# Optimization experiments

Hardware: AMD Instinct MI355X
Metric: run time of the kernel (lower is better)

Reference implementation:

```python
import jax, jax.numpy as jnp
import numpy as np

K = 3          # kernel_size
DIL = 2        # dilation
PAD = 2        # padding = dilation*(K-1)/2 so output spatial == input spatial
RANKS = 3
EPS = 1e-6


def _unfold(h):
    """Replicate-pad then extract KxK dilated patches -> (b, c, K*K, H, W).
    Kernel-position ordering matches torch.nn.Unfold (row-major kh*K+kw)."""
    b, c, H, W = h.shape
    p = jnp.pad(h, ((0, 0), (0, 0), (PAD, PAD), (PAD, PAD)), mode='edge')
    patches = [p[:, :, i * DIL:i * DIL + H, j * DIL:j * DIL + W]
               for i in range(K) for j in range(K)]
    return jnp.stack(patches, axis=2)  # (b, c, K*K, H, W)


def setup_inputs() -> dict:
    key = jax.random.key(0)
    k1, k2, k3 = jax.random.split(key, 3)
    B, C, H, W = 4, 64, 128, 128
    x = jax.random.normal(k1, (B, C, H, W), dtype=jnp.float32)
    W_head = jax.random.normal(k2, (64, 64), dtype=jnp.float32) * 0.05  # (out_c, in_c)
    W_tail = jax.random.normal(k3, (64, 64), dtype=jnp.float32) * 0.05  # (in_c, out_c)
    return {"x": x, "W_head": W_head, "W_tail": W_tail}


def reference(x, W_head, W_tail):
    res = x
    # 1x1 head conv (no bias) + ReLU
    h = jax.nn.relu(jnp.einsum('oc,bchw->bohw', W_head, x))
    # im2col: (b, C, K*K, H, W)
    X = _unfold(h)
    # NMF-style init: broadcast means over kernel / channel dims to rank r
    U = jnp.repeat(X.mean(axis=2, keepdims=True), RANKS, axis=2)  # (b,c,r,h,w)
    V = jnp.repeat(X.mean(axis=1, keepdims=True), RANKS, axis=1)  # (b,r,k,h,w)
    # one Lee-Seung multiplicative update (stage_num=1)
    num = jnp.einsum('bcrhw,bckhw->brkhw', U, X)
    den = jnp.einsum('bcrhw,bckhw->brkhw', U,
                     jnp.einsum('bcrhw,brkhw->bckhw', U, V))
    V = V * (num / (den + EPS))
    num = jnp.einsum('bckhw,brkhw->bcrhw', X, V)
    den = jnp.einsum('bckhw,brkhw->bcrhw',
                     jnp.einsum('bcrhw,brkhw->bckhw', U, V), V)
    U = U * (num / (den + EPS))
    center = (K // 2) * K + K // 2  # = 4
    UV = jnp.einsum('bcrhw,brkhw->bckhw', U, V[:, :, center:center + 1])[:, :, 0]
    out = jnp.einsum('co,bohw->bchw', W_tail, UV) + res
    return out
```

## Files before the change

### kernel.cpp

```cpp
#include <hip/hip_runtime.h>
#include <hip/hip_bf16.h>

#define HWC 16384
#define WD  128
#define NC  64
#define EPSV 1e-6f

typedef __attribute__((ext_vector_type(8))) short bf16x8;
typedef __attribute__((ext_vector_type(4))) float f32x4;
typedef __attribute__((ext_vector_type(2))) float f32x2;
typedef __attribute__((ext_vector_type(4))) unsigned int u32x4;

__device__ __forceinline__ unsigned cvt2(float a, float b) {
  union { __hip_bfloat162 h; unsigned u; } r;
  r.h = __float22bfloat162_rn(make_float2(a, b));
  return r.u;
}
__device__ __forceinline__ float bfLo(unsigned pk) { return __builtin_bit_cast(float, pk << 16); }
__device__ __forceinline__ float bfHi(unsigned pk) { return __builtin_bit_cast(float, pk & 0xFFFF0000u); }
__device__ __forceinline__ f32x2 up2(unsigned w) {
  f32x2 r; r[0] = bfLo(w); r[1] = bfHi(w); return r;
}
__device__ __forceinline__ float frcp(float x) { return __builtin_amdgcn_rcpf(x); }
__device__ __forceinline__ int swz(int row, int colbytes) {
  return ((row << 7) + colbytes) ^ ((row & 7) << 4);
}
__device__ __forceinline__ bf16x8 pack8(float4 a, float4 b) {
  union { unsigned u[4]; bf16x8 v; } r;
  r.u[0] = cvt2(a.x, a.y); r.u[1] = cvt2(a.z, a.w);
  r.u[2] = cvt2(b.x, b.y); r.u[3] = cvt2(b.z, b.w);
  return r.v;
}

__global__ __launch_bounds__(512) void k_fused(const float* __restrict__ x,
                                               const float* __restrict__ Wh,
                                               const float* __restrict__ Wt,
                                               float* __restrict__ out) {
  __shared__ __align__(16) char smem[53248];
  unsigned short* xt = (unsigned short*)smem;
  unsigned short* hl = (unsigned short*)(smem + 26624);
  unsigned short* uvb = (unsigned short*)smem;

  const int t = threadIdx.x, lane = t & 63, wv = t >> 6;
  const int bid0 = blockIdx.x;
  const int bid = ((bid0 & 7) << 7) | (bid0 >> 3);
  const int seg = bid & 1, y = (bid >> 1) & 127, b = bid >> 8;
  const int w0 = seg << 6;
  const int c0 = wv << 3;
  const int l15 = lane & 15, kg = lane >> 4;
  const int mt = wv & 3;
  const int mrow = (mt << 4) + l15;

  int gy[3];
  gy[0] = y >= 2 ? y - 2 : 0;
  gy[1] = y;
  gy[2] = y <= 125 ? y + 2 : 127;

  const float* xb = x + (size_t)b * (NC * HWC);

  bf16x8 ha0, ha1;
  {
    const float* wr = Wh + mrow * 64 + kg * 8;
    ha0 = pack8(*(const float4*)wr, *(const float4*)(wr + 4));
    ha1 = pack8(*(const float4*)(wr + 32), *(const float4*)(wr + 36));
  }

  {
    int colm = w0 - 2 + lane; if (colm < 0) colm = 0;
#pragma unroll
    for (int r = 0; r < 3; ++r) {
      const float* xr = xb + gy[r] * WD + colm;
      float f[8];
#pragma unroll
      for (int u = 0; u < 8; ++u) f[u] = xr[(size_t)(c0 + u) * HWC];
      u32x4 v;
      v[0] = cvt2(f[0], f[1]); v[1] = cvt2(f[2], f[3]);
      v[2] = cvt2(f[4], f[5]); v[3] = cvt2(f[6], f[7]);
      *(u32x4*)((char*)xt + swz(r * 68 + lane, c0 * 2)) = v;
    }
    if (lane < 12) {
      const int re = lane >> 2, e = lane & 3;
      int cole = w0 + 62 + e; if (cole > 127) cole = 127;
      const float* xr = xb + gy[re] * WD + cole;
      float f[8];
#pragma unroll
      for (int u = 0; u < 8; ++u) f[u] = xr[(size_t)(c0 + u) * HWC];
      u32x4 v;
      v[0] = cvt2(f[0], f[1]); v[1] = cvt2(f[2], f[3]);
      v[2] = cvt2(f[4], f[5]); v[3] = cvt2(f[6], f[7]);
      *(u32x4*)((char*)xt + swz(re * 68 + 64 + e, c0 * 2)) = v;
    }
  }
  __syncthreads();

  {
    const int ntBeg = (wv >> 2) ? 7 : 0;
    const int ntEnd = (wv >> 2) ? 13 : 7;
    const f32x4 z = {0.f, 0.f, 0.f, 0.f};
    for (int nt = ntBeg; nt < ntEnd; ++nt) {
      const int s = (nt << 4) + l15;
      const bf16x8 b0 = *(const bf16x8*)((char*)xt + swz(s, kg * 16));
      const bf16x8 b1 = *(const bf16x8*)((char*)xt + swz(s, 64 + kg * 16));
      f32x4 acc = __builtin_amdgcn_mfma_f32_16x16x32_bf16(ha0, b0, z, 0, 0, 0);
      acc = __builtin_amdgcn_mfma_f32_16x16x32_bf16(ha1, b1, acc, 0, 0, 0);
      const float v0 = acc[0] > 0.f ? acc[0] : 0.f;
      const float v1 = acc[1] > 0.f ? acc[1] : 0.f;
      const float v2 = acc[2] > 0.f ? acc[2] : 0.f;
      const float v3 = acc[3] > 0.f ? acc[3] : 0.f;
      uint2 pk2;
      pk2.x = cvt2(v0, v1);
      pk2.y = cvt2(v2, v3);
      *(uint2*)((char*)hl + swz(s, (mt * 16 + kg * 4) * 2)) = pk2;
    }
  }
  __syncthreads();

  const int px = (wv << 3) | (lane >> 3);
  const int cg16 = (lane & 7) << 4;

  u32x4 tap[9];
#pragma unroll
  for (int r = 0; r < 3; ++r)
#pragma unroll
    for (int kc = 0; kc < 3; ++kc)
      tap[r * 3 + kc] = *(const u32x4*)((char*)hl + swz(r * 68 + px + 2 * kc, cg16));

  f32x2 S2 = {0.f, 0.f};
  f32x2 sumk2[9], A2[9], mreg2[4];
#pragma unroll
  for (int k = 0; k < 9; ++k) { sumk2[k] = (f32x2){0.f, 0.f}; A2[k] = (f32x2){0.f, 0.f}; }
#pragma unroll
  for (int p = 0; p < 4; ++p) {
    f32x2 t2[9];
#pragma unroll
    for (int k = 0; k < 9; ++k) t2[k] = up2(tap[k][p]);
    f32x2 mm = t2[0];
#pragma unroll
    for (int k = 1; k < 9; ++k) mm += t2[k];
    mm *= (1.f / 9.f);
    mreg2[p] = mm;
    S2 += mm * mm;
#pragma unroll
    for (int k = 0; k < 9; ++k) { sumk2[k] += t2[k]; A2[k] += mm * t2[k]; }
  }
  float S = S2[0] + S2[1];
  float sumk[9], A[9];
#pragma unroll
  for (int k = 0; k < 9; ++k) { sumk[k] = sumk2[k][0] + sumk2[k][1]; A[k] = A2[k][0] + A2[k][1]; }

#pragma unroll
  for (int d = 1; d <= 4; d <<= 1) {
    S += __shfl_xor(S, d);
#pragma unroll
    for (int k = 0; k < 9; ++k) sumk[k] += __shfl_xor(sumk[k], d);
#pragma unroll
    for (int k = 0; k < 9; ++k) A[k] += __shfl_xor(A[k], d);
  }

  float Vk[9], T = 0.f;
#pragma unroll
  for (int k = 0; k < 9; ++k) {
    const float nk = sumk[k] * (1.f / 64.f);
    Vk[k] = nk * A[k] * frcp(3.f * nk * S + EPSV);
    T += Vk[k] * Vk[k];
  }
  const float V4 = Vk[4];

  bf16x8 ta0, ta1;
  {
    const float* wr = Wt + mrow * 64 + kg * 8;
    ta0 = pack8(*(const float4*)wr, *(const float4*)(wr + 4));
    ta1 = pack8(*(const float4*)(wr + 32), *(const float4*)(wr + 36));
  }

  {
    u32x4 uvw;
#pragma unroll
    for (int p = 0; p < 4; ++p) {
      f32x2 B2 = {0.f, 0.f};
#pragma unroll
      for (int k = 0; k < 9; ++k) B2 += up2(tap[k][p]) * Vk[k];
      const f32x2 mm = mreg2[p];
      f32x2 rden;
      rden[0] = frcp(3.f * mm[0] * T + EPSV);
      rden[1] = frcp(3.f * mm[1] * T + EPSV);
      const f32x2 Uc = mm * B2 * rden;
      const f32x2 uvv = 3.f * Uc * V4;
      uvw[p] = cvt2(uvv[0], uvv[1]);
    }
    *(u32x4*)((char*)uvb + swz(px, cg16)) = uvw;
  }
  __syncthreads();

  const int n0 = (wv >> 2) << 1;
  const f32x4 z2 = {0.f, 0.f, 0.f, 0.f};
  const size_t gb = (size_t)b * (NC * HWC) + (size_t)y * WD + w0;
#pragma unroll
  for (int nt = n0; nt < n0 + 2; ++nt) {
    const int pxs = (nt << 4) + l15;
    const bf16x8 b0 = *(const bf16x8*)((char*)uvb + swz(pxs, kg * 16));
    const bf16x8 b1 = *(const bf16x8*)((char*)uvb + swz(pxs, 64 + kg * 16));
    f32x4 acc = __builtin_amdgcn_mfma_f32_16x16x32_bf16(ta0, b0, z2, 0, 0, 0);
    acc = __builtin_amdgcn_mfma_f32_16x16x32_bf16(ta1, b1, acc, 0, 0, 0);
#pragma unroll
    for (int j = 0; j < 4; ++j) {
      const int c2 = (mt << 4) + kg * 4 + j;
      const size_t off = gb + (size_t)c2 * HWC + pxs;
      out[off] = acc[j] + x[off];
    }
  }
}

extern "C" void kernel_launch(void* const* d_in, const int* in_sizes, int n_in,
                              void* d_out, int out_size, void* d_ws, size_t ws_size,
                              hipStream_t stream) {
  const float* x  = (const float*)d_in[0];
  const float* Wh = (const float*)d_in[1];
  const float* Wt = (const float*)d_in[2];
  float* out = (float*)d_out;

  k_fused<<<1024, 512, 0, stream>>>(x, Wh, Wt, out);
}
```

Before: 24.15 us.

## Tile four output rows per block with double-buffered row staging

Each block now computes a 4-row by 32-column tile instead of one 64-wide row. It stages the 8 needed input rows one at a time into double-buffered LDS and runs the head 1x1 conv per row while the next row loads. This cuts redundant recomputation of the head conv for halo rows: it is computed 8 times per 4 outputs instead of 3 times per output. In exchange the halo overhead in width grows, there are more barriers and a serialized row loop, the launch drops to 512 blocks of 256 threads, and the ragged-tile handling adds some wasted MFMA work.

```diff
diff --git a/kernel.cpp b/kernel.cpp
--- a/kernel.cpp
+++ b/kernel.cpp
@@ -32,29 +32,59 @@
   return r.v;
 }
 
-__global__ __launch_bounds__(512) void k_fused(const float* __restrict__ x,
+__device__ __forceinline__ void stage_row(const float* __restrict__ xr, int w0,
+                                          int t, unsigned short* buf) {
+  {
+    const int s = t & 31, cg = t >> 5;
+    int col = w0 - 2 + s; if (col < 0) col = 0;
+    const float* p = xr + col;
+    float f[8];
+#pragma unroll
+    for (int u = 0; u < 8; ++u) f[u] = p[(size_t)(cg * 8 + u) * HWC];
+    u32x4 v;
+    v[0] = cvt2(f[0], f[1]); v[1] = cvt2(f[2], f[3]);
+    v[2] = cvt2(f[4], f[5]); v[3] = cvt2(f[6], f[7]);
+    *(u32x4*)((char*)buf + swz(s, cg * 16)) = v;
+  }
+  if (t < 32) {
+    const int s = 32 + (t & 3), cg = t >> 2;
+    int col = w0 - 2 + s; if (col > 127) col = 127;
+    const float* p = xr + col;
+    float f[8];
+#pragma unroll
+    for (int u = 0; u < 8; ++u) f[u] = p[(size_t)(cg * 8 + u) * HWC];
+    u32x4 v;
+    v[0] = cvt2(f[0], f[1]); v[1] = cvt2(f[2], f[3]);
+    v[2] = cvt2(f[4], f[5]); v[3] = cvt2(f[6], f[7]);
+    *(u32x4*)((char*)buf + swz(s, cg * 16)) = v;
+  }
+}
+
+__global__ __launch_bounds__(256) void k_fused(const float* __restrict__ x,
                                                const float* __restrict__ Wh,
                                                const float* __restrict__ Wt,
                                                float* __restrict__ out) {
-  __shared__ __align__(16) char smem[53248];
-  unsigned short* xt = (unsigned short*)smem;
-  unsigned short* hl = (unsigned short*)(smem + 26624);
+  __shared__ __align__(16) char smem[49152];
+  unsigned short* bufA = (unsigned short*)smem;
+  unsigned short* bufB = (unsigned short*)(smem + 6144);
+  unsigned short* hl = (unsigned short*)(smem + 12288);
   unsigned short* uvb = (unsigned short*)smem;
 
   const int t = threadIdx.x, lane = t & 63, wv = t >> 6;
   const int bid0 = blockIdx.x;
-  const int bid = ((bid0 & 7) << 7) | (bid0 >> 3);
-  const int seg = bid & 1, y = (bid >> 1) & 127, b = bid >> 8;
-  const int w0 = seg << 6;
-  const int c0 = wv << 3;
+  const int bidS = ((bid0 & 7) << 6) | (bid0 >> 3);
+  const int seg = bidS & 3, yq = (bidS >> 2) & 31, b = bidS >> 7;
+  const int w0 = seg << 5;
+  const int y0 = yq << 2;
   const int l15 = lane & 15, kg = lane >> 4;
-  const int mt = wv & 3;
-  const int mrow = (mt << 4) + l15;
-
-  int gy[3];
-  gy[0] = y >= 2 ? y - 2 : 0;
-  gy[1] = y;
-  gy[2] = y <= 125 ? y + 2 : 127;
+  const int mrow = (wv << 4) + l15;
+
+  int gyw[8];
+#pragma unroll
+  for (int i = 0; i < 8; ++i) {
+    int yy = y0 - 2 + i;
+    gyw[i] = yy < 0 ? 0 : (yy > 127 ? 127 : yy);
+  }
 
   const float* xb = x + (size_t)b * (NC * HWC);
 
@@ -65,106 +95,36 @@
     ha1 = pack8(*(const float4*)(wr + 32), *(const float4*)(wr + 36));
   }
 
-  {
-    int colm = w0 - 2 + lane; if (colm < 0) colm = 0;
-#pragma unroll
-    for (int r = 0; r < 3; ++r) {
-      const float* xr = xb + gy[r] * WD + colm;
-      float f[8];
-#pragma unroll
-      for (int u = 0; u < 8; ++u) f[u] = xr[(size_t)(c0 + u) * HWC];
-      u32x4 v;
-      v[0] = cvt2(f[0], f[1]); v[1] = cvt2(f[2], f[3]);
-      v[2] = cvt2(f[4], f[5]); v[3] = cvt2(f[6], f[7]);
-      *(u32x4*)((char*)xt + swz(r * 68 + lane, c0 * 2)) = v;
-    }
-    if (lane < 12) {
-      const int re = lane >> 2, e = lane & 3;
-      int cole = w0 + 62 + e; if (cole > 127) cole = 127;
-      const float* xr = xb + gy[re] * WD + cole;
-      float f[8];
-#pragma unroll
-      for (int u = 0; u < 8; ++u) f[u] = xr[(size_t)(c0 + u) * HWC];
-      u32x4 v;
-      v[0] = cvt2(f[0], f[1]); v[1] = cvt2(f[2], f[3]);
-      v[2] = cvt2(f[4], f[5]); v[3] = cvt2(f[6], f[7]);
-      *(u32x4*)((char*)xt + swz(re * 68 + 64 + e, c0 * 2)) = v;
-    }
-  }
+  stage_row(xb + gyw[0] * WD, w0, t, bufA);
   __syncthreads();
-
-  {
-    const int ntBeg = (wv >> 2) ? 7 : 0;
-    const int ntEnd = (wv >> 2) ? 13 : 7;
-    const f32x4 z = {0.f, 0.f, 0.f, 0.f};
-    for (int nt = ntBeg; nt < ntEnd; ++nt) {
-      const int s = (nt << 4) + l15;
-      const bf16x8 b0 = *(const bf16x8*)((char*)xt + swz(s, kg * 16));
-      const bf16x8 b1 = *(const bf16x8*)((char*)xt + swz(s, 64 + kg * 16));
-      f32x4 acc = __builtin_amdgcn_mfma_f32_16x16x32_bf16(ha0, b0, z, 0, 0, 0);
-      acc = __builtin_amdgcn_mfma_f32_16x16x32_bf16(ha1, b1, acc, 0, 0, 0);
-      const float v0 = acc[0] > 0.f ? acc[0] : 0.f;
-      const float v1 = acc[1] > 0.f ? acc[1] : 0.f;
-      const float v2 = acc[2] > 0.f ? acc[2] : 0.f;
-      const float v3 = acc[3] > 0.f ? acc[3] : 0.f;
-      uint2 pk2;
-      pk2.x = cvt2(v0, v1);
-      pk2.y = cvt2(v2, v3);
-      *(uint2*)((char*)hl + swz(s, (mt * 16 + kg * 4) * 2)) = pk2;
-    }
-  }
-  __syncthreads();
-
-  const int px = (wv << 3) | (lane >> 3);
-  const int cg16 = (lane & 7) << 4;
-
-  u32x4 tap[9];
-#pragma unroll
-  for (int r = 0; r < 3; ++r)
-#pragma unroll
-    for (int kc = 0; kc < 3; ++kc)
-      tap[r * 3 + kc] = *(const u32x4*)((char*)hl + swz(r * 68 + px + 2 * kc, cg16));
-
-  f32x2 S2 = {0.f, 0.f};
-  f32x2 sumk2[9], A2[9], mreg2[4];
-#pragma unroll
-  for (int k = 0; k < 9; ++k) { sumk2[k] = (f32x2){0.f, 0.f}; A2[k] = (f32x2){0.f, 0.f}; }
-#pragma unroll
-  for (int p = 0; p < 4; ++p) {
-    f32x2 t2[9];
-#pragma unroll
-    for (int k = 0; k < 9; ++k) t2[k] = up2(tap[k][p]);
-    f32x2 mm = t2[0];
-#pragma unroll
-    for (int k = 1; k < 9; ++k) mm += t2[k];
-    mm *= (1.f / 9.f);
-    mreg2[p] = mm;
-    S2 += mm * mm;
-#pragma unroll
-    for (int k = 0; k < 9; ++k) { sumk2[k] += t2[k]; A2[k] += mm * t2[k]; }
-  }
-  float S = S2[0] + S2[1];
-  float sumk[9], A[9];
-#pragma unroll
-  for (int k = 0; k < 9; ++k) { sumk[k] = sumk2[k][0] + sumk2[k][1]; A[k] = A2[k][0] + A2[k][1]; }
-
-#pragma unroll
-  for (int d = 1; d <= 4; d <<= 1) {
-    S += __shfl_xor(S, d);
-#pragma unroll
-    for (int k = 0; k < 9; ++k) sumk[k] += __shfl_xor(sumk[k], d);
-#pragma unroll
-    for (int k = 0; k < 9; ++k) A[k] += __shfl_xor(A[k], d);
-  }
-
-  float Vk[9], T = 0.f;
-#pragma unroll
-  for (int k = 0; k < 9; ++k) {
-    const float nk = sumk[k] * (1.f / 64.f);
-    Vk[k] = nk * A[k] * frcp(3.f * nk * S + EPSV);
-    T += Vk[k] * Vk[k];
-  }
-  const float V4 = Vk[4];
+#pragma unroll
+  for (int r = 0; r < 8; ++r) {
+    unsigned short* cur = (r & 1) ? bufB : bufA;
+    unsigned short* nxt = (r & 1) ? bufA : bufB;
+    if (r < 7) stage_row(xb + gyw[r + 1] * WD, w0, t, nxt);
+    {
+      const f32x4 zz = {0.f, 0.f, 0.f, 0.f};
+#pragma unroll
+      for (int nt = 0; nt < 3; ++nt) {
+        const int s = (nt << 4) + l15;
+        const bf16x8 b0 = *(const bf16x8*)((char*)cur + swz(s, kg * 16));
+        const bf16x8 b1 = *(const bf16x8*)((char*)cur + swz(s, 64 + kg * 16));
+        f32x4 acc = __builtin_amdgcn_mfma_f32_16x16x32_bf16(ha0, b0, zz, 0, 0, 0);
+        acc = __builtin_amdgcn_mfma_f32_16x16x32_bf16(ha1, b1, acc, 0, 0, 0);
+        if (s < 36) {
+          const float v0 = acc[0] > 0.f ? acc[0] : 0.f;
+          const float v1 = acc[1] > 0.f ? acc[1] : 0.f;
+          const float v2 = acc[2] > 0.f ? acc[2] : 0.f;
+          const float v3 = acc[3] > 0.f ? acc[3] : 0.f;
+          uint2 pk2;
+          pk2.x = cvt2(v0, v1);
+          pk2.y = cvt2(v2, v3);
+          *(uint2*)((char*)hl + swz(r * 36 + s, (wv * 16 + kg * 4) * 2)) = pk2;
+        }
+      }
+    }
+    __syncthreads();
+  }
 
   bf16x8 ta0, ta1;
   {
@@ -173,41 +133,97 @@
     ta1 = pack8(*(const float4*)(wr + 32), *(const float4*)(wr + 36));
   }
 
-  {
-    u32x4 uvw;
+  const int px = (wv << 3) | (lane >> 3);
+  const int cg16 = (lane & 7) << 4;
+
+#pragma unroll
+  for (int q = 0; q < 4; ++q) {
+    u32x4 tap[9];
+#pragma unroll
+    for (int rr = 0; rr < 3; ++rr)
+#pragma unroll
+      for (int kc = 0; kc < 3; ++kc)
+        tap[rr * 3 + kc] =
+            *(const u32x4*)((char*)hl + swz((q + 2 * rr) * 36 + px + 2 * kc, cg16));
+
+    f32x2 S2 = {0.f, 0.f};
+    f32x2 sumk2[9], A2[9], mreg2[4];
+#pragma unroll
+    for (int k = 0; k < 9; ++k) { sumk2[k] = (f32x2){0.f, 0.f}; A2[k] = (f32x2){0.f, 0.f}; }
 #pragma unroll
     for (int p = 0; p < 4; ++p) {
-      f32x2 B2 = {0.f, 0.f};
-#pragma unroll
-      for (int k = 0; k < 9; ++k) B2 += up2(tap[k][p]) * Vk[k];
-      const f32x2 mm = mreg2[p];
-      f32x2 rden;
-      rden[0] = frcp(3.f * mm[0] * T + EPSV);
-      rden[1] = frcp(3.f * mm[1] * T + EPSV);
-      const f32x2 Uc = mm * B2 * rden;
-      const f32x2 uvv = 3.f * Uc * V4;
-      uvw[p] = cvt2(uvv[0], uvv[1]);
-    }
-    *(u32x4*)((char*)uvb + swz(px, cg16)) = uvw;
-  }
-  __syncthreads();
-
-  const int n0 = (wv >> 2) << 1;
-  const f32x4 z2 = {0.f, 0.f, 0.f, 0.f};
-  const size_t gb = (size_t)b * (NC * HWC) + (size_t)y * WD + w0;
-#pragma unroll
-  for (int nt = n0; nt < n0 + 2; ++nt) {
-    const int pxs = (nt << 4) + l15;
-    const bf16x8 b0 = *(const bf16x8*)((char*)uvb + swz(pxs, kg * 16));
-    const bf16x8 b1 = *(const bf16x8*)((char*)uvb + swz(pxs, 64 + kg * 16));
-    f32x4 acc = __builtin_amdgcn_mfma_f32_16x16x32_bf16(ta0, b0, z2, 0, 0, 0);
-    acc = __builtin_amdgcn_mfma_f32_16x16x32_bf16(ta1, b1, acc, 0, 0, 0);
-#pragma unroll
-    for (int j = 0; j < 4; ++j) {
-      const int c2 = (mt << 4) + kg * 4 + j;
-      const size_t off = gb + (size_t)c2 * HWC + pxs;
-      out[off] = acc[j] + x[off];
-    }
+      f32x2 t2[9];
+#pragma unroll
+      for (int k = 0; k < 9; ++k) t2[k] = up2(tap[k][p]);
+      f32x2 mm = t2[0];
+#pragma unroll
+      for (int k = 1; k < 9; ++k) mm += t2[k];
+      mm *= (1.f / 9.f);
+      mreg2[p] = mm;
+      S2 += mm * mm;
+#pragma unroll
+      for (int k = 0; k < 9; ++k) { sumk2[k] += t2[k]; A2[k] += mm * t2[k]; }
+    }
+    float S = S2[0] + S2[1];
+    float sumk[9], A[9];
+#pragma unroll
+    for (int k = 0; k < 9; ++k) { sumk[k] = sumk2[k][0] + sumk2[k][1]; A[k] = A2[k][0] + A2[k][1]; }
+
+#pragma unroll
+    for (int d = 1; d <= 4; d <<= 1) {
+      S += __shfl_xor(S, d);
+#pragma unroll
+      for (int k = 0; k < 9; ++k) sumk[k] += __shfl_xor(sumk[k], d);
+#pragma unroll
+      for (int k = 0; k < 9; ++k) A[k] += __shfl_xor(A[k], d);
+    }
+
+    float Vk[9], T = 0.f;
+#pragma unroll
+    for (int k = 0; k < 9; ++k) {
+      const float nk = sumk[k] * (1.f / 64.f);
+      Vk[k] = nk * A[k] * frcp(3.f * nk * S + EPSV);
+      T += Vk[k] * Vk[k];
+    }
+    const float V4 = Vk[4];
+
+    {
+      u32x4 uvw;
+#pragma unroll
+      for (int p = 0; p < 4; ++p) {
+        f32x2 B2 = {0.f, 0.f};
+#pragma unroll
+        for (int k = 0; k < 9; ++k) B2 += up2(tap[k][p]) * Vk[k];
+        const f32x2 mm = mreg2[p];
+        f32x2 rden;
+        rden[0] = frcp(3.f * mm[0] * T + EPSV);
+        rden[1] = frcp(3.f * mm[1] * T + EPSV);
+        const f32x2 Uc = mm * B2 * rden;
+        const f32x2 uvv = 3.f * Uc * V4;
+        uvw[p] = cvt2(uvv[0], uvv[1]);
+      }
+      *(u32x4*)((char*)uvb + swz(px, cg16)) = uvw;
+    }
+    __syncthreads();
+
+    const int Y = y0 + q;
+    const f32x4 z2 = {0.f, 0.f, 0.f, 0.f};
+    const size_t gb = (size_t)b * (NC * HWC) + (size_t)Y * WD + w0;
+#pragma unroll
+    for (int nt = 0; nt < 2; ++nt) {
+      const int pxs = (nt << 4) + l15;
+      const bf16x8 b0 = *(const bf16x8*)((char*)uvb + swz(pxs, kg * 16));
+      const bf16x8 b1 = *(const bf16x8*)((char*)uvb + swz(pxs, 64 + kg * 16));
+      f32x4 acc = __builtin_amdgcn_mfma_f32_16x16x32_bf16(ta0, b0, z2, 0, 0, 0);
+      acc = __builtin_amdgcn_mfma_f32_16x16x32_bf16(ta1, b1, acc, 0, 0, 0);
+#pragma unroll
+      for (int j = 0; j < 4; ++j) {
+        const int c2 = (wv << 4) + kg * 4 + j;
+        const size_t off = gb + (size_t)c2 * HWC + pxs;
+        out[off] = acc[j] + x[off];
+      }
+    }
+    __syncthreads();
   }
 }
 
@@ -219,5 +235,5 @@
   const float* Wt = (const float*)d_in[2];
   float* out = (float*)d_out;
 
-  k_fused<<<1024, 512, 0, stream>>>(x, Wh, Wt, out);
-}
+  k_fused<<<512, 256, 0, stream>>>(x, Wh, Wt, out);
+}
```

Measured after the change: 27.02 us. 1.12x slower.
